# Kernel optimization log

Measured on AMD Instinct MI355X. Metric: run time of the kernel, lower is better.

Reference implementation:

```python
import jax, jax.numpy as jnp
import numpy as np

UNITS = 2048
D_IN = 96
BATCH = 64
T = 512
C_IN = 10        # connectivity_input: nnz per input-kernel row
C_REC = 10       # connectivity_recurrent: nnz per recurrent-kernel column
INPUT_SCALING = 1.0
SPECTRAL_RADIUS = 0.99
LEAKY = 1.0


def setup_inputs() -> dict:
    rng = np.random.default_rng(0)
    # --- input kernel: sparse (D_IN, UNITS), C_IN nonzeros per row (COO) ---
    krows = np.repeat(np.arange(D_IN), C_IN).astype(np.int32)                 # [D_IN*C_IN]
    kcols = np.stack([rng.choice(UNITS, size=C_IN, replace=False)
                      for _ in range(D_IN)]).reshape(-1).astype(np.int32)
    kvals = (2.0 * (2.0 * rng.random(D_IN * C_IN) - 1.0)).astype(np.float32) * np.float32(INPUT_SCALING)
    # --- recurrent kernel: sparse (UNITS, UNITS), C_REC nonzeros per column ---
    # rec_idx[i, j] = source row feeding output unit (column) i
    rec_idx = np.stack([rng.choice(UNITS, size=C_REC, replace=False)
                        for _ in range(UNITS)]).astype(np.int32)              # [UNITS, C_REC]
    rec_vals = (2.0 * (2.0 * rng.random((UNITS, C_REC)) - 1.0)).astype(np.float32)
    # spectral-radius normalization via exact eigenvalues (matches tf.linalg.eig path, leaky==1)
    W = np.zeros((UNITS, UNITS), np.float32)
    W[rec_idx.reshape(-1), np.repeat(np.arange(UNITS), C_REC)] = rec_vals.reshape(-1)
    rho = np.abs(np.linalg.eigvals(W)).max()
    rec_vals = rec_vals * np.float32(SPECTRAL_RADIUS / rho)
    # --- bias ---
    bias = (2.0 * rng.random(UNITS) - 1.0).astype(np.float32) * np.float32(INPUT_SCALING)
    key = jax.random.key(0)
    inputs = jax.random.normal(key, (BATCH, T, D_IN), dtype=jnp.float32)
    state0 = jnp.zeros((BATCH, UNITS), dtype=jnp.float32)
    return {
        "inputs": inputs,
        "state0": state0,
        "kernel_vals": jnp.asarray(kvals),
        "rec_vals": jnp.asarray(rec_vals),
        "bias": jnp.asarray(bias),
        "kernel_rows": jnp.asarray(krows),
        "kernel_cols": jnp.asarray(kcols),
        "rec_idx": jnp.asarray(rec_idx),
    }


def reference(inputs, state0, kernel_vals, rec_vals, bias, kernel_rows, kernel_cols, rec_idx):
    units = bias.shape[0]

    def step(h, x_t):                                     # h: [B, units], x_t: [B, D_IN]
        # input_part = x_t @ kernel (sparse COO, fixed degree per row)
        contrib = x_t[:, kernel_rows] * kernel_vals       # [B, nnz_in]
        input_part = jax.ops.segment_sum(contrib.T, kernel_cols, num_segments=units).T  # [B, units]
        # state_part = h @ W (fixed C_REC sources per output unit -> gather+reduce)
        state_part = jnp.einsum('bnc,nc->bn', h[:, rec_idx], rec_vals)  # [B, units]
        h_new = h * (1.0 - LEAKY) + jnp.tanh(input_part + bias + state_part) * LEAKY
        return h_new, h_new

    _, ys = jax.lax.scan(step, state0, jnp.swapaxes(inputs, 0, 1))  # ys: [T, B, units]
    return jnp.swapaxes(ys, 0, 1)                                   # [B, T, units]
```

## Files before the change

### kernel.cpp

```cpp
#include <hip/hip_runtime.h>

namespace {
constexpr int UNITS = 2048;
constexpr int D_IN  = 96;
constexpr int BATCH = 64;
constexpr int T     = 512;
constexpr int NNZ   = 960;
constexpr int C_REC = 10;
constexpr int CHUNK = 128;
constexpr int NT    = 1024;

constexpr int HA = 0;
constexpr int HB = 8192;
constexpr int IA = 16384;
constexpr int IB = 24576;
constexpr int XO = 32768;
constexpr int LDS_BYTES = XO + CHUNK * D_IN * 4;
}

typedef float f32x2 __attribute__((ext_vector_type(2)));

__device__ __forceinline__ void bar_lds() {
  asm volatile("s_waitcnt lgkmcnt(0)\n\ts_barrier" ::: "memory");
}

__device__ __forceinline__ float fast_tanh(float x) {
  float e = __expf(2.0f * x);
  return 1.0f - __fdividef(2.0f, e + 1.0f);
}

#define REC_DECL(n)                                          \
  const int   ia##n = ridx[u0 * C_REC + n] * 4;              \
  const int   ib##n = ridx[u0 * C_REC + C_REC + n] * 4;      \
  const float wa##n = rvals[u0 * C_REC + n];                 \
  const float wb##n = rvals[u0 * C_REC + C_REC + n];

#define GATHER(HC, n)                                        \
  s0 += *(const float*)(smem + (HC) + ia##n) * wa##n;        \
  s1 += *(const float*)(smem + (HC) + ib##n) * wb##n;

#define STEP(HC, HN, IR, IW, SLOT_NEXT, DO_SCATTER, TSTEP)                     \
  {                                                                            \
    if ((DO_SCATTER) && tid < NNZ) {                                           \
      float xv = *(const float*)(smem + XO + (SLOT_NEXT) * (D_IN * 4) + krb);  \
      atomicAdd((float*)(smem + (IW) + kcb), xv * kv);                         \
    }                                                                          \
    f32x2 in2 = *(f32x2*)(smem + (IR) + tid * 8);                              \
    *(f32x2*)(smem + (IR) + tid * 8) = (f32x2){0.f, 0.f};                      \
    float s0 = in2.x + bias2.x;                                                \
    float s1 = in2.y + bias2.y;                                                \
    GATHER(HC, 0) GATHER(HC, 1) GATHER(HC, 2) GATHER(HC, 3) GATHER(HC, 4)      \
    GATHER(HC, 5) GATHER(HC, 6) GATHER(HC, 7) GATHER(HC, 8) GATHER(HC, 9)      \
    f32x2 hh = {fast_tanh(s0), fast_tanh(s1)};                                 \
    *(f32x2*)(smem + (HN) + tid * 8) = hh;                                     \
    __builtin_nontemporal_store(hh, outp + (size_t)(TSTEP) * (UNITS / 2));     \
    bar_lds();                                                                 \
  }

__global__ __launch_bounds__(NT, 4) void reservoir_kernel(
    const float* __restrict__ inputs, const float* __restrict__ state0,
    const float* __restrict__ kvals,  const float* __restrict__ rvals,
    const float* __restrict__ bias,   const int* __restrict__ krows,
    const int* __restrict__ kcols,    const int* __restrict__ ridx,
    float* __restrict__ out)
{
  __shared__ __align__(16) char smem[LDS_BYTES];
  const int tid = threadIdx.x;
  const int b   = blockIdx.x;
  const int u0  = tid * 2;

  *(float4*)(smem + IA + tid * 16) = make_float4(0.f, 0.f, 0.f, 0.f);
  *(f32x2*)(smem + HA + tid * 8) = *(const f32x2*)(state0 + b * UNITS + u0);

  REC_DECL(0) REC_DECL(1) REC_DECL(2) REC_DECL(3) REC_DECL(4)
  REC_DECL(5) REC_DECL(6) REC_DECL(7) REC_DECL(8) REC_DECL(9)

  const f32x2 bias2 = *(const f32x2*)(bias + u0);

  int krb = 0, kcb = 0; float kv = 0.f;
  if (tid < NNZ) {
    krb = krows[tid] * 4;
    kcb = kcols[tid] * 4;
    kv  = kvals[tid];
  }

  const float* xin  = inputs + (size_t)b * (T * D_IN);
  f32x2*       outp = (f32x2*)out + (size_t)b * (T * (UNITS / 2)) + tid;

  __syncthreads();

  for (int tb = 0; tb < T; tb += CHUNK) {
#pragma unroll
    for (int k = 0; k < 3; ++k) {
      float4 v = *(const float4*)(xin + tb * D_IN + (tid + k * NT) * 4);
      *(float4*)(smem + XO + (tid + k * NT) * 16) = v;
    }
    bar_lds();
    if (tid < NNZ) {
      float xv = *(const float*)(smem + XO + krb);
      atomicAdd((float*)(smem + IA + kcb), xv * kv);
    }
    bar_lds();
#pragma unroll 1
    for (int ts = 0; ts < CHUNK; ts += 2) {
      STEP(HA, HB, IA, IB, ts + 1, true,              tb + ts);
      STEP(HB, HA, IB, IA, ts + 2, (ts + 2) < CHUNK,  tb + ts + 1);
    }
  }
}

extern "C" void kernel_launch(void* const* d_in, const int* in_sizes, int n_in,
                              void* d_out, int out_size, void* d_ws, size_t ws_size,
                              hipStream_t stream) {
  const float* inputs = (const float*)d_in[0];
  const float* state0 = (const float*)d_in[1];
  const float* kvals  = (const float*)d_in[2];
  const float* rvals  = (const float*)d_in[3];
  const float* bias   = (const float*)d_in[4];
  const int*   krows  = (const int*)d_in[5];
  const int*   kcols  = (const int*)d_in[6];
  const int*   ridx   = (const int*)d_in[7];

  reservoir_kernel<<<dim3(BATCH), dim3(NT), 0, stream>>>(
      inputs, state0, kvals, rvals, bias, krows, kcols, ridx, (float*)d_out);
}
```

Measured before the change: 1.256 ms.

## Halve block threads, duplicate state copies and schedule gathers to avoid LDS bank conflicts

```diff
diff --git a/kernel.cpp b/kernel.cpp
--- a/kernel.cpp
+++ b/kernel.cpp
@@ -7,18 +7,20 @@
 constexpr int T     = 512;
 constexpr int NNZ   = 960;
 constexpr int C_REC = 10;
-constexpr int CHUNK = 128;
-constexpr int NT    = 1024;
+constexpr int NTH   = 512;
 
 constexpr int HA = 0;
-constexpr int HB = 8192;
-constexpr int IA = 16384;
-constexpr int IB = 24576;
-constexpr int XO = 32768;
-constexpr int LDS_BYTES = XO + CHUNK * D_IN * 4;
-}
-
-typedef float f32x2 __attribute__((ext_vector_type(2)));
+constexpr int HB = 16384;
+constexpr int IA = 32768;
+constexpr int IB = 40960;
+constexpr int LDS_BYTES = 49152;
+
+constexpr int OFFS_OFS = 0;
+constexpr int WTAB_OFS = 40 * NTH * 4;
+constexpr int WS_NEED  = 80 * NTH * 4;
+}
+
+typedef float f32x4 __attribute__((ext_vector_type(4)));
 
 __device__ __forceinline__ void bar_lds() {
   asm volatile("s_waitcnt lgkmcnt(0)\n\ts_barrier" ::: "memory");
@@ -29,83 +31,147 @@
   return 1.0f - __fdividef(2.0f, e + 1.0f);
 }
 
-#define REC_DECL(n)                                          \
-  const int   ia##n = ridx[u0 * C_REC + n] * 4;              \
-  const int   ib##n = ridx[u0 * C_REC + C_REC + n] * 4;      \
-  const float wa##n = rvals[u0 * C_REC + n];                 \
-  const float wb##n = rvals[u0 * C_REC + C_REC + n];
-
-#define GATHER(HC, n)                                        \
-  s0 += *(const float*)(smem + (HC) + ia##n) * wa##n;        \
-  s1 += *(const float*)(smem + (HC) + ib##n) * wb##n;
-
-#define STEP(HC, HN, IR, IW, SLOT_NEXT, DO_SCATTER, TSTEP)                     \
+__global__ __launch_bounds__(64) void prep_sched(
+    const int* __restrict__ ridx, const float* __restrict__ rvals,
+    int* __restrict__ offs, float* __restrict__ wtab)
+{
+  const int w = blockIdx.x, l = threadIdx.x;
+  __shared__ int   sidx[256 * C_REC];
+  __shared__ float sval[256 * C_REC];
+  __shared__ int   hist[32];
+  for (int i = l; i < 256 * C_REC; i += 64) {
+    sidx[i] = ridx[w * 256 * C_REC + i];
+    sval[i] = rvals[w * 256 * C_REC + i];
+  }
+  __syncthreads();
+  const int tidm = w * 64 + l;
+  unsigned rem0 = 0x3FF, rem1 = 0x3FF, rem2 = 0x3FF, rem3 = 0x3FF;
+
+#define SLOT(LU, K)                                                            \
   {                                                                            \
-    if ((DO_SCATTER) && tid < NNZ) {                                           \
-      float xv = *(const float*)(smem + XO + (SLOT_NEXT) * (D_IN * 4) + krb);  \
-      atomicAdd((float*)(smem + (IW) + kcb), xv * kv);                         \
+    if (l < 32) hist[l] = 0;                                                   \
+    __syncthreads();                                                           \
+    unsigned m = rem##LU;                                                      \
+    const int nc = 2 * __popc(m);                                              \
+    int pe = -1, pc = 0, pidx = 0;                                             \
+    for (int r = 0; r < 6 && pe < 0; ++r) {                                    \
+      const int rr = (r < nc) ? r : (r % nc);                                  \
+      const int er = rr >> 1, cp = rr & 1;                                     \
+      int cnt = 0, ce = 0;                                                     \
+      _Pragma("unroll")                                                        \
+      for (int e = 0; e < C_REC; ++e)                                          \
+        if ((m >> e) & 1) { if (cnt == er) ce = e; ++cnt; }                    \
+      const int idx  = sidx[(4 * l + LU) * C_REC + ce];                        \
+      const int bank = (idx + 8 * cp) & 31;                                    \
+      const int old  = atomicAdd(&hist[bank], 1);                              \
+      if (old < 2 || r == 5) { pe = ce; pc = cp; pidx = idx; }                 \
+      else atomicSub(&hist[bank], 1);                                          \
     }                                                                          \
-    f32x2 in2 = *(f32x2*)(smem + (IR) + tid * 8);                              \
-    *(f32x2*)(smem + (IR) + tid * 8) = (f32x2){0.f, 0.f};                      \
-    float s0 = in2.x + bias2.x;                                                \
-    float s1 = in2.y + bias2.y;                                                \
-    GATHER(HC, 0) GATHER(HC, 1) GATHER(HC, 2) GATHER(HC, 3) GATHER(HC, 4)      \
-    GATHER(HC, 5) GATHER(HC, 6) GATHER(HC, 7) GATHER(HC, 8) GATHER(HC, 9)      \
-    f32x2 hh = {fast_tanh(s0), fast_tanh(s1)};                                 \
-    *(f32x2*)(smem + (HN) + tid * 8) = hh;                                     \
-    __builtin_nontemporal_store(hh, outp + (size_t)(TSTEP) * (UNITS / 2));     \
+    rem##LU = m & ~(1u << pe);                                                 \
+    offs[((LU) * C_REC + (K)) * NTH + tidm] =                                  \
+        pc * 8192 + ((pidx + 8 * pc) & 2047) * 4;                              \
+    wtab[((LU) * C_REC + (K)) * NTH + tidm] = sval[(4 * l + LU) * C_REC + pe]; \
+    __syncthreads();                                                           \
+  }
+
+#define SLOT10(LU)                                                             \
+  SLOT(LU, 0) SLOT(LU, 1) SLOT(LU, 2) SLOT(LU, 3) SLOT(LU, 4)                  \
+  SLOT(LU, 5) SLOT(LU, 6) SLOT(LU, 7) SLOT(LU, 8) SLOT(LU, 9)
+
+  SLOT10(0) SLOT10(1) SLOT10(2) SLOT10(3)
+#undef SLOT10
+#undef SLOT
+}
+
+#define RDECL(LU, K)                                                           \
+  const int   o##LU##_##K = PERM ? offs[((LU) * C_REC + (K)) * NTH + tid]      \
+                                 : ridx[(u0 + (LU)) * C_REC + (K)] * 4;        \
+  const float w##LU##_##K = PERM ? wtab[((LU) * C_REC + (K)) * NTH + tid]      \
+                                 : rvals[(u0 + (LU)) * C_REC + (K)];
+#define RDECL10(LU)                                                            \
+  RDECL(LU, 0) RDECL(LU, 1) RDECL(LU, 2) RDECL(LU, 3) RDECL(LU, 4)             \
+  RDECL(LU, 5) RDECL(LU, 6) RDECL(LU, 7) RDECL(LU, 8) RDECL(LU, 9)
+
+#define GAT(HC, LU, K)                                                         \
+  s##LU += *(const float*)(smem + (HC) + o##LU##_##K) * w##LU##_##K;
+#define GAT10(HC, LU)                                                          \
+  GAT(HC, LU, 0) GAT(HC, LU, 1) GAT(HC, LU, 2) GAT(HC, LU, 3) GAT(HC, LU, 4)   \
+  GAT(HC, LU, 5) GAT(HC, LU, 6) GAT(HC, LU, 7) GAT(HC, LU, 8) GAT(HC, LU, 9)
+
+#define STEP(HC, HN, IR, IW, DO_SCATTER, TSTEP)                                \
+  {                                                                            \
+    f32x4 in4 = *(f32x4*)(smem + (IR) + tid * 16);                             \
+    *(f32x4*)(smem + (IR) + tid * 16) = (f32x4){0.f, 0.f, 0.f, 0.f};           \
+    float s0 = in4.x + bias4.x, s1 = in4.y + bias4.y;                          \
+    float s2 = in4.z + bias4.z, s3 = in4.w + bias4.w;                          \
+    GAT10(HC, 0) GAT10(HC, 1) GAT10(HC, 2) GAT10(HC, 3)                        \
+    if (DO_SCATTER) {                                                          \
+      atomicAdd((float*)(smem + (IW) + c1), x1 * v1);                          \
+      if (e2) atomicAdd((float*)(smem + (IW) + c2), x2 * v2);                  \
+    }                                                                          \
+    f32x4 hh = {fast_tanh(s0), fast_tanh(s1), fast_tanh(s2), fast_tanh(s3)};   \
+    *(f32x4*)(smem + (HN) + pb0) = hh;                                         \
+    *(f32x4*)(smem + (HN) + pb1) = hh;                                         \
+    __builtin_nontemporal_store(hh, outp + (size_t)(TSTEP) * (UNITS / 4));     \
+    {                                                                          \
+      int tnx = (TSTEP) + 2 < T ? (TSTEP) + 2 : T - 1;                         \
+      x1 = xin[tnx * D_IN + r1];                                               \
+      if (e2) x2 = xin[tnx * D_IN + r2];                                       \
+    }                                                                          \
     bar_lds();                                                                 \
   }
 
-__global__ __launch_bounds__(NT, 4) void reservoir_kernel(
+template <bool PERM>
+__global__ __launch_bounds__(NTH, 2) void reservoir_kernel(
     const float* __restrict__ inputs, const float* __restrict__ state0,
     const float* __restrict__ kvals,  const float* __restrict__ rvals,
     const float* __restrict__ bias,   const int* __restrict__ krows,
     const int* __restrict__ kcols,    const int* __restrict__ ridx,
+    const int* __restrict__ offs,     const float* __restrict__ wtab,
     float* __restrict__ out)
 {
   __shared__ __align__(16) char smem[LDS_BYTES];
   const int tid = threadIdx.x;
   const int b   = blockIdx.x;
-  const int u0  = tid * 2;
-
-  *(float4*)(smem + IA + tid * 16) = make_float4(0.f, 0.f, 0.f, 0.f);
-  *(f32x2*)(smem + HA + tid * 8) = *(const f32x2*)(state0 + b * UNITS + u0);
-
-  REC_DECL(0) REC_DECL(1) REC_DECL(2) REC_DECL(3) REC_DECL(4)
-  REC_DECL(5) REC_DECL(6) REC_DECL(7) REC_DECL(8) REC_DECL(9)
-
-  const f32x2 bias2 = *(const f32x2*)(bias + u0);
-
-  int krb = 0, kcb = 0; float kv = 0.f;
-  if (tid < NNZ) {
-    krb = krows[tid] * 4;
-    kcb = kcols[tid] * 4;
-    kv  = kvals[tid];
-  }
+  const int u0  = 4 * tid;
+
+  const int pb0 = u0 * 4;
+  const int pb1 = 8192 + ((u0 + 8) & 2047) * 4;
+
+  *(f32x4*)(smem + IA + tid * 16) = (f32x4){0.f, 0.f, 0.f, 0.f};
+  *(f32x4*)(smem + IB + tid * 16) = (f32x4){0.f, 0.f, 0.f, 0.f};
+  f32x4 h0 = *(const f32x4*)(state0 + b * UNITS + u0);
+  *(f32x4*)(smem + HA + pb0) = h0;
+  *(f32x4*)(smem + HA + pb1) = h0;
+
+  RDECL10(0) RDECL10(1) RDECL10(2) RDECL10(3)
+
+  const f32x4 bias4 = *(const f32x4*)(bias + u0);
+
+  const bool e2 = tid < NNZ - NTH;
+  const int   r1 = krows[tid];
+  const int   c1 = kcols[tid] * 4;
+  const float v1 = kvals[tid];
+  const int   r2 = e2 ? krows[NTH + tid] : 0;
+  const int   c2 = e2 ? kcols[NTH + tid] * 4 : 0;
+  const float v2 = e2 ? kvals[NTH + tid] : 0.f;
 
   const float* xin  = inputs + (size_t)b * (T * D_IN);
-  f32x2*       outp = (f32x2*)out + (size_t)b * (T * (UNITS / 2)) + tid;
-
+  f32x4*       outp = (f32x4*)out + (size_t)b * (T * (UNITS / 4)) + tid;
+
+  float x1 = xin[r1];
+  float x2 = e2 ? xin[r2] : 0.f;
   __syncthreads();
-
-  for (int tb = 0; tb < T; tb += CHUNK) {
-#pragma unroll
-    for (int k = 0; k < 3; ++k) {
-      float4 v = *(const float4*)(xin + tb * D_IN + (tid + k * NT) * 4);
-      *(float4*)(smem + XO + (tid + k * NT) * 16) = v;
-    }
-    bar_lds();
-    if (tid < NNZ) {
-      float xv = *(const float*)(smem + XO + krb);
-      atomicAdd((float*)(smem + IA + kcb), xv * kv);
-    }
-    bar_lds();
+  atomicAdd((float*)(smem + IA + c1), x1 * v1);
+  if (e2) atomicAdd((float*)(smem + IA + c2), x2 * v2);
+  x1 = xin[D_IN + r1];
+  if (e2) x2 = xin[D_IN + r2];
+  bar_lds();
+
 #pragma unroll 1
-    for (int ts = 0; ts < CHUNK; ts += 2) {
-      STEP(HA, HB, IA, IB, ts + 1, true,              tb + ts);
-      STEP(HB, HA, IB, IA, ts + 2, (ts + 2) < CHUNK,  tb + ts + 1);
-    }
+  for (int ts = 0; ts < T; ts += 2) {
+    STEP(HA, HB, IA, IB, true,         ts);
+    STEP(HB, HA, IB, IA, (ts + 2) < T, ts + 1);
   }
 }
 
@@ -121,6 +187,17 @@
   const int*   kcols  = (const int*)d_in[6];
   const int*   ridx   = (const int*)d_in[7];
 
-  reservoir_kernel<<<dim3(BATCH), dim3(NT), 0, stream>>>(
-      inputs, state0, kvals, rvals, bias, krows, kcols, ridx, (float*)d_out);
-}
+  int*   offs = (int*)((char*)d_ws + OFFS_OFS);
+  float* wtab = (float*)((char*)d_ws + WTAB_OFS);
+
+  if (ws_size >= (size_t)WS_NEED) {
+    prep_sched<<<dim3(8), dim3(64), 0, stream>>>(ridx, rvals, offs, wtab);
+    reservoir_kernel<true><<<dim3(BATCH), dim3(NTH), 0, stream>>>(
+        inputs, state0, kvals, rvals, bias, krows, kcols, ridx, offs, wtab,
+        (float*)d_out);
+  } else {
+    reservoir_kernel<false><<<dim3(BATCH), dim3(NTH), 0, stream>>>(
+        inputs, state0, kvals, rvals, bias, krows, kcols, ridx, offs, wtab,
+        (float*)d_out);
+  }
+}
```

Measured after the change: 1.203 ms. 4.2% less time.
